# Performance work log

Measured on AMD Instinct MI355X. Metric: run time of the kernel, lower is better.

The kernel has to match this reference:

```python
import jax, jax.numpy as jnp
import numpy as np

B, S, HID = 1, 4096, 2048
HQ, HKV, D = 16, 8, 128
G = HQ // HKV
WINDOW = 1024
EPS = 1e-6
ROPE_THETA = 1e6


def setup_inputs() -> dict:
    key = jax.random.key(0)
    ks = jax.random.split(key, 6)
    hidden_states = jax.random.normal(ks[0], (B, S, HID), dtype=jnp.float32)
    Wq = jax.random.normal(ks[1], (HQ * D, HID), dtype=jnp.float32) * 0.02
    Wk = jax.random.normal(ks[2], (HKV * D, HID), dtype=jnp.float32) * 0.02
    Wv = jax.random.normal(ks[3], (HKV * D, HID), dtype=jnp.float32) * 0.02
    Wo = jax.random.normal(ks[4], (HID, HQ * D), dtype=jnp.float32) * 0.02
    q_norm_w = jnp.ones((D,), dtype=jnp.float32)
    k_norm_w = jnp.ones((D,), dtype=jnp.float32)
    # standard RoPE tables
    inv_freq = 1.0 / (ROPE_THETA ** (jnp.arange(0, D, 2, dtype=jnp.float32) / D))
    pos = jnp.arange(S, dtype=jnp.float32)
    freqs = pos[:, None] * inv_freq[None, :]            # [S, D/2]
    emb = jnp.concatenate([freqs, freqs], axis=-1)       # [S, D]
    cos = jnp.cos(emb)[None]                             # [1, S, D]
    sin = jnp.sin(emb)[None]
    return {"hidden_states": hidden_states, "cos": cos, "sin": sin,
            "Wq": Wq, "Wk": Wk, "Wv": Wv, "Wo": Wo,
            "q_norm_w": q_norm_w, "k_norm_w": k_norm_w}


def _rms_norm(x, w):
    var = jnp.mean(jnp.square(x), axis=-1, keepdims=True)
    return w * (x * jax.lax.rsqrt(var + EPS))


def _rotate_half(x):
    x1, x2 = jnp.split(x, 2, axis=-1)
    return jnp.concatenate([-x2, x1], axis=-1)


def reference(hidden_states, cos, sin, Wq, Wk, Wv, Wo, q_norm_w, k_norm_w):
    b, s, _ = hidden_states.shape
    # projections -> [B, H, S, D]
    q = (hidden_states @ Wq.T).reshape(b, s, HQ, D)
    k = (hidden_states @ Wk.T).reshape(b, s, HKV, D)
    v = (hidden_states @ Wv.T).reshape(b, s, HKV, D)
    q = _rms_norm(q, q_norm_w).transpose(0, 2, 1, 3)   # [B,HQ,S,D]
    k = _rms_norm(k, k_norm_w).transpose(0, 2, 1, 3)   # [B,HKV,S,D]
    v = v.transpose(0, 2, 1, 3)
    # RoPE (cos/sin broadcast over head dim)
    c = cos[:, None, :, :]
    sn = sin[:, None, :, :]
    q = q * c + _rotate_half(q) * sn
    k = k * c + _rotate_half(k) * sn
    # GQA: group queries per kv head
    qg = q.reshape(b, HKV, G, s, D)
    scaling = D ** -0.5
    scores = jnp.einsum('bhgqd,bhkd->bhgqk', qg, k) * scaling  # [B,HKV,G,S,S]
    # causal + sliding-window additive mask
    i = jnp.arange(s)[:, None]
    j = jnp.arange(s)[None, :]
    allowed = (j <= i) & (j > i - WINDOW)
    scores = jnp.where(allowed[None, None, None], scores, jnp.float32(-1e9))
    attn = jax.nn.softmax(scores, axis=-1)
    out = jnp.einsum('bhgqk,bhkd->bhgqd', attn, v)     # [B,HKV,G,S,D]
    out = out.reshape(b, HQ, s, D).transpose(0, 2, 1, 3).reshape(b, s, HQ * D)
    return out @ Wo.T
```

## Files before the change

### kernel.cpp

```cpp
#include <hip/hip_runtime.h>

typedef __bf16 bf16;
typedef bf16 bf16x8 __attribute__((ext_vector_type(8)));
typedef bf16 bf16x4 __attribute__((ext_vector_type(4)));
typedef float f32x4 __attribute__((ext_vector_type(4)));

#define MFMA16(a, b, c) __builtin_amdgcn_mfma_f32_16x16x32_bf16((a), (b), (c), 0, 0, 0)

__device__ __forceinline__ void gload_lds16(const bf16* g, bf16* l) {
  __builtin_amdgcn_global_load_lds(
      (const __attribute__((address_space(1))) void*)g,
      (__attribute__((address_space(3))) void*)l, 16, 0, 0);
}

template <int N>
__device__ __forceinline__ void lgkm_fence() {
  if constexpr (N == 0) asm volatile("s_waitcnt lgkmcnt(0)" ::: "memory");
  else if constexpr (N == 4) asm volatile("s_waitcnt lgkmcnt(4)" ::: "memory");
  else if constexpr (N == 8) asm volatile("s_waitcnt lgkmcnt(8)" ::: "memory");
  else if constexpr (N == 12) asm volatile("s_waitcnt lgkmcnt(12)" ::: "memory");
  __builtin_amdgcn_sched_barrier(0);
}
__device__ __forceinline__ void bar_fence() {
  __builtin_amdgcn_sched_barrier(0);
  __builtin_amdgcn_s_barrier();
}

__global__ __launch_bounds__(256) void cvt_f32_bf16(const float* __restrict__ src,
                                                    bf16* __restrict__ dst, int n4) {
  int i = blockIdx.x * blockDim.x + threadIdx.x;
  if (i < n4) {
    float4 v = ((const float4*)src)[i];
    bf16x4 o;
    o[0] = (bf16)v.x; o[1] = (bf16)v.y; o[2] = (bf16)v.z; o[3] = (bf16)v.w;
    ((bf16x4*)dst)[i] = o;
  }
}

template <int BM, int BN, int MT, int NTT, typename OutT>
__global__ __launch_bounds__(512, 2) void gemm_pipe(const bf16* __restrict__ A,
                                                    const bf16* __restrict__ B,
                                                    OutT* __restrict__ C,
                                                    int M, int N, int K) {
  constexpr int MH = MT / 2, NH = NTT / 2;
  constexpr int ASLOT = BM * 64;
  constexpr int BSLOT = BN * 64;
  constexpr int NLA = BM / 64, NLB = BN / 64;
  __shared__ __align__(16) bf16 SA[2 * ASLOT];
  __shared__ __align__(16) bf16 SB[2 * BSLOT];

  const int NTILES = K >> 6;
  const int tid = threadIdx.x;
  const int w = tid >> 6, lane = tid & 63;
  const int l15 = lane & 15, quad = lane >> 4;
  const int wr = w >> 2, wc = w & 3;

  const int nbx = N / BN;
  const int nwg = (M / BM) * nbx;
  const int wg = ((int)blockIdx.x & 7) * (nwg >> 3) + ((int)blockIdx.x >> 3);
  const int bm0 = (wg / nbx) * BM;
  const int bn0 = (wg % nbx) * BN;

  const int r0 = tid >> 3;
  const int sg = (tid & 7) ^ ((tid >> 3) & 7);
  unsigned aoffg[NLA], boffg[NLB];
#pragma unroll
  for (int i = 0; i < NLA; ++i)
    aoffg[i] = (unsigned)((bm0 + r0 + i * 64) * K + sg * 8);
#pragma unroll
  for (int i = 0; i < NLB; ++i)
    boffg[i] = (unsigned)((bn0 + r0 + i * 64) * K + sg * 8);

  const int xl = l15 & 7;
  const int p0 = quad ^ xl;
  const int baseA0 = (wr * (MT * 16) + l15) * 128 + p0 * 16;
  const int baseA1 = (wr * (MT * 16) + l15) * 128 + ((p0 ^ 4) * 16);
  const int baseB0 = (wc * (NTT * 16) + l15) * 128 + p0 * 16;
  const int baseB1 = (wc * (NTT * 16) + l15) * 128 + ((p0 ^ 4) * 16);
  const char* saB = (const char*)&SA[0];
  const char* sbB = (const char*)&SB[0];

  f32x4 acc[MT][NTT] = {};
  bf16x8 As[2][MH][2];
  bf16x8 Bs[2][NH][2];

#define LDA_(SL, H, DST)                                                        \
  _Pragma("unroll") for (int mt = 0; mt < MH; ++mt) {                           \
    (DST)[mt][0] = *(const bf16x8*)(saB + (SL) * (ASLOT * 2) + baseA0 +         \
                                    ((H) * MH + mt) * 2048);                    \
    (DST)[mt][1] = *(const bf16x8*)(saB + (SL) * (ASLOT * 2) + baseA1 +         \
                                    ((H) * MH + mt) * 2048);                    \
  }
#define LDB_(SL, G, DST)                                                        \
  _Pragma("unroll") for (int nt = 0; nt < NH; ++nt) {                           \
    (DST)[nt][0] = *(const bf16x8*)(sbB + (SL) * (BSLOT * 2) + baseB0 +         \
                                    ((G) * NH + nt) * 2048);                    \
    (DST)[nt][1] = *(const bf16x8*)(sbB + (SL) * (BSLOT * 2) + baseB1 +         \
                                    ((G) * NH + nt) * 2048);                    \
  }
#define QMFMA_(AS, BS, MHI, NHI)                                                \
  __builtin_amdgcn_s_setprio(1);                                                \
  _Pragma("unroll") for (int mt = 0; mt < MH; ++mt)                             \
      _Pragma("unroll") for (int nt = 0; nt < NH; ++nt) {                       \
    acc[(MHI) * MH + mt][(NHI) * NH + nt] = MFMA16(                             \
        (AS)[mt][0], (BS)[nt][0], acc[(MHI) * MH + mt][(NHI) * NH + nt]);       \
    acc[(MHI) * MH + mt][(NHI) * NH + nt] = MFMA16(                             \
        (AS)[mt][1], (BS)[nt][1], acc[(MHI) * MH + mt][(NHI) * NH + nt]);       \
  }                                                                             \
  __builtin_amdgcn_s_setprio(0);
#define STAGE_(SO, TS)                                                          \
  _Pragma("unroll") for (int i = 0; i < NLA; ++i)                               \
      gload_lds16(A + aoffg[i] + (TS) * 64, SA + (SO) * ASLOT + tid * 8 + i * 4096); \
  _Pragma("unroll") for (int i = 0; i < NLB; ++i)                               \
      gload_lds16(B + boffg[i] + (TS) * 64, SB + (SO) * BSLOT + tid * 8 + i * 4096);

#define GTILE_BODY(PAR, TS)                                                     \
  {                                                                             \
    constexpr int sl_ = (PAR), so_ = (PAR) ^ 1;                                 \
    constexpr int e0_ = (PAR), e1_ = (PAR) ^ 1;                                 \
                                                                        \
    LDB_(sl_, 1, Bs[e1_]);                                                      \
    bar_fence();                                                                \
    lgkm_fence<NTT>();                                                          \
    if ((TS) < NTILES) { STAGE_(so_, (TS)); }                                   \
    QMFMA_(As[0], Bs[e0_], 0, 0);                                               \
                                                                        \
    LDA_(sl_, 1, As[1]);                                                        \
    bar_fence();                                                                \
    lgkm_fence<MT>();                                                           \
    QMFMA_(As[0], Bs[e1_], 0, 1);                                               \
                                                                        \
    LDB_(sl_, 0, Bs[e0_]);                                                      \
    asm volatile("s_waitcnt vmcnt(0)" ::: "memory");                            \
    bar_fence();                                                                \
    lgkm_fence<NTT>();                                                          \
    QMFMA_(As[1], Bs[e1_], 1, 1);                                               \
                                                                        \
    LDA_(so_, 0, As[0]);                                                        \
    LDB_(so_, 0, Bs[e1_]);                                                      \
    bar_fence();                                                                \
    lgkm_fence<MT + NTT>();                                                     \
    QMFMA_(As[1], Bs[e0_], 1, 0);                                               \
  }

  { STAGE_(0, 0); }
  asm volatile("s_waitcnt vmcnt(0)" ::: "memory");
  bar_fence();
  __builtin_amdgcn_sched_barrier(0);
  LDA_(0, 0, As[0]);
  LDB_(0, 0, Bs[0]);

  for (int t = 0; t < NTILES; t += 2) {
    GTILE_BODY(0, t + 1);
    GTILE_BODY(1, t + 2);
  }

#undef LDA_
#undef LDB_
#undef QMFMA_
#undef STAGE_
#undef GTILE_BODY

#pragma unroll
  for (int mt = 0; mt < MT; ++mt)
#pragma unroll
    for (int nt = 0; nt < NTT; ++nt) {
      int row = bm0 + wr * (MT * 16) + mt * 16 + quad * 4;
      int col = bn0 + wc * (NTT * 16) + nt * 16 + l15;
#pragma unroll
      for (int r = 0; r < 4; ++r)
        C[(size_t)(row + r) * N + col] = (OutT)acc[mt][nt][r];
    }
}

__global__ __launch_bounds__(256) void normrope(const bf16* __restrict__ QKVb,
                                                const float* __restrict__ cosb,
                                                const float* __restrict__ sinb,
                                                const float* __restrict__ qw,
                                                const float* __restrict__ kw,
                                                bf16* __restrict__ Qb,
                                                bf16* __restrict__ Kb) {
  const int wid = (blockIdx.x * blockDim.x + threadIdx.x) >> 6;
  const int lane = threadIdx.x & 63;
  const int s = wid / 24;
  const int h = wid % 24;
  const bool isq = (h < 16);
  const int col0 = isq ? h * 128 : 2048 + (h - 16) * 128;
  const float* wt = isq ? qw : kw;

  const bf16* row = QKVb + (size_t)s * 4096 + col0;
  float x1 = (float)row[lane];
  float x2 = (float)row[lane + 64];

  float ss = x1 * x1 + x2 * x2;
#pragma unroll
  for (int m = 32; m >= 1; m >>= 1) ss += __shfl_xor(ss, m, 64);
  float rs = rsqrtf(ss * (1.0f / 128.0f) + 1e-6f);

  float c = cosb[(size_t)s * 128 + lane];
  float sn = sinb[(size_t)s * 128 + lane];
  float xn1 = x1 * rs * wt[lane];
  float xn2 = x2 * rs * wt[lane + 64];
  float o1 = xn1 * c - xn2 * sn;
  float o2 = xn2 * c + xn1 * sn;
  const float scale = isq ? 0.12751652f : 1.0f;
  o1 *= scale; o2 *= scale;

  bf16* dst = isq ? (Qb + ((size_t)h * 4096 + s) * 128)
                  : (Kb + ((size_t)(h - 16) * 4096 + s) * 128);
  dst[lane] = (bf16)o1;
  dst[lane + 64] = (bf16)o2;
}

__global__ __launch_bounds__(256) void vtrans(const bf16* __restrict__ QKVb,
                                              bf16* __restrict__ Vtp) {
  __shared__ __align__(16) bf16 T[64 * 136];
  const int kvh = blockIdx.y;
  const int s0 = blockIdx.x * 64;
  const int tid = threadIdx.x;
  for (int g = tid; g < 1024; g += 256) {
    int s = g >> 4, cg = g & 15;
    *(bf16x8*)(T + s * 136 + cg * 8) =
        *(const bf16x8*)(QKVb + (size_t)(s0 + s) * 4096 + 3072 + kvh * 128 + cg * 8);
  }
  __syncthreads();
  for (int g = tid; g < 1024; g += 256) {
    int d = g >> 3, sg = g & 7;
    bf16x8 v;
#pragma unroll
    for (int j = 0; j < 8; j++) {
      int kp = sg * 8 + j;
      int s = (kp & 3) * 16 + (kp >> 2);
      v[j] = T[s * 136 + d];
    }
    *(bf16x8*)(Vtp + ((size_t)kvh * 128 + d) * 4096 + s0 + sg * 8) = v;
  }
}

__global__ __launch_bounds__(256, 2) void attn_kernel(const bf16* __restrict__ Qb,
                                                      const bf16* __restrict__ Kb,
                                                      const bf16* __restrict__ Vtp,
                                                      bf16* __restrict__ Ob) {
  const int SEQ = 4096, W = 1024;
  const float MP = 17.312340f;
  __shared__ __align__(16) bf16 Ks[64 * 128];
  __shared__ __align__(16) bf16 Vs[128 * 64];
  __shared__ __align__(16) bf16 Ps[4][32 * 64];

  const int id = blockIdx.x;
  const int kvh = id & 7, gq = (id >> 3) & 1, h = kvh * 2 + gq;
  const int qb0 = (id >> 4) * 128;
  const int tid = threadIdx.x, w = tid >> 6, lane = tid & 63;
  const int l15 = lane & 15, quad = lane >> 4;
  const int qw0 = qb0 + w * 32;

  bf16x8 qf[2][4];
#pragma unroll
  for (int m = 0; m < 2; m++) {
    const bf16* qp = Qb + ((size_t)h * SEQ + qw0 + m * 16 + l15) * 128 + quad * 8;
#pragma unroll
    for (int kb = 0; kb < 4; kb++) qf[m][kb] = *(const bf16x8*)(qp + kb * 32);
  }

  f32x4 o[2][8] = {};
  f32x4 lr[2] = {};
  bf16* pw = &Ps[w][0];
  const bf16* kbase = Kb + (size_t)kvh * SEQ * 128;
  const bf16* vbase = Vtp + (size_t)kvh * 128 * SEQ;

  int jmin = qb0 - (W - 1); if (jmin < 0) jmin = 0;
  const int kt0 = jmin >> 6, kt1 = (qb0 + 127) >> 6;

  for (int kt = kt0; kt <= kt1; ++kt) {
    const int k0 = kt * 64;
#pragma unroll
    for (int i = 0; i < 4; i++) {
      int slot = w * 256 + i * 64 + lane;
      int key = slot >> 4, gg = slot & 15;
      int gsw = gg ^ (key & 7);
      gload_lds16(kbase + (size_t)(k0 + key) * 128 + gsw * 8, Ks + (w * 256 + i * 64) * 8);
    }
#pragma unroll
    for (int i = 0; i < 4; i++) {
      int slot = w * 256 + i * 64 + lane;
      int d = slot >> 3, gg = slot & 7;
      int gsw = gg ^ (d & 7);
      gload_lds16(vbase + (size_t)d * SEQ + k0 + gsw * 8, Vs + (w * 256 + i * 64) * 8);
    }
    __syncthreads();

    const bool alive = (k0 <= qw0 + 31) && (k0 + 63 > qw0 - W);
    if (alive) {
      const bool full = (k0 + 63 <= qw0) && (k0 > qw0 + 31 - W);
      f32x4 s[2][4] = {};
#pragma unroll
      for (int c = 0; c < 4; c++) {
        const int key = c * 16 + l15;
        bf16x8 kf[4];
#pragma unroll
        for (int kb = 0; kb < 4; kb++)
          kf[kb] = *(const bf16x8*)(Ks + key * 128 + (((kb * 4 + quad) ^ (key & 7)) << 3));
#pragma unroll
        for (int kb = 0; kb < 4; kb++) {
          s[0][c] = MFMA16(qf[0][kb], kf[kb], s[0][c]);
          s[1][c] = MFMA16(qf[1][kb], kf[kb], s[1][c]);
        }
      }
#pragma unroll
      for (int m = 0; m < 2; m++)
#pragma unroll
        for (int r = 0; r < 4; r++) {
          float p[4];
          if (full) {
#pragma unroll
            for (int c = 0; c < 4; c++) p[c] = __builtin_amdgcn_exp2f(s[m][c][r] - MP);
          } else {
            const int i_ = qw0 + m * 16 + quad * 4 + r;
#pragma unroll
            for (int c = 0; c < 4; c++) {
              int j = k0 + c * 16 + l15;
              p[c] = (j <= i_ && j > i_ - W) ? __builtin_amdgcn_exp2f(s[m][c][r] - MP) : 0.0f;
            }
          }
          lr[m][r] += p[0] + p[1] + p[2] + p[3];
          bf16x4 pk;
          pk[0] = (bf16)p[0]; pk[1] = (bf16)p[1]; pk[2] = (bf16)p[2]; pk[3] = (bf16)p[3];
          const int qrow = m * 16 + quad * 4 + r;
          *(bf16x4*)(pw + qrow * 64 + (((l15 >> 1) ^ (qrow & 7)) << 3) + (l15 & 1) * 4) = pk;
        }
      asm volatile("s_waitcnt lgkmcnt(0)" ::: "memory");
      bf16x8 pf[2][2];
#pragma unroll
      for (int m = 0; m < 2; m++)
#pragma unroll
        for (int kb = 0; kb < 2; kb++)
          pf[m][kb] = *(const bf16x8*)(pw + (m * 16 + l15) * 64 +
                                       (((kb * 4 + quad) ^ (l15 & 7)) << 3));
#pragma unroll
      for (int n = 0; n < 8; n++) {
        const int d = n * 16 + l15;
        bf16x8 vf0 = *(const bf16x8*)(Vs + d * 64 + ((quad ^ (l15 & 7)) << 3));
        bf16x8 vf1 = *(const bf16x8*)(Vs + d * 64 + (((4 + quad) ^ (l15 & 7)) << 3));
        o[0][n] = MFMA16(pf[0][0], vf0, o[0][n]);
        o[0][n] = MFMA16(pf[0][1], vf1, o[0][n]);
        o[1][n] = MFMA16(pf[1][0], vf0, o[1][n]);
        o[1][n] = MFMA16(pf[1][1], vf1, o[1][n]);
      }
    }
    __syncthreads();
  }

  float linv[2][4];
#pragma unroll
  for (int m = 0; m < 2; m++)
#pragma unroll
    for (int r = 0; r < 4; r++) {
      float v = lr[m][r];
      v += __shfl_xor(v, 1, 64);
      v += __shfl_xor(v, 2, 64);
      v += __shfl_xor(v, 4, 64);
      v += __shfl_xor(v, 8, 64);
      linv[m][r] = 1.0f / v;
    }
#pragma unroll
  for (int m = 0; m < 2; m++)
#pragma unroll
    for (int n = 0; n < 8; n++)
#pragma unroll
      for (int r = 0; r < 4; r++) {
        int i_ = qw0 + m * 16 + quad * 4 + r;
        Ob[(size_t)i_ * 2048 + h * 128 + n * 16 + l15] = (bf16)(o[m][n][r] * linv[m][r]);
      }
}

extern "C" void kernel_launch(void* const* d_in, const int* in_sizes, int n_in,
                              void* d_out, int out_size, void* d_ws, size_t ws_size,
                              hipStream_t stream) {
  const float* hid  = (const float*)d_in[0];
  const float* cosb = (const float*)d_in[1];
  const float* sinb = (const float*)d_in[2];
  const float* Wq   = (const float*)d_in[3];
  const float* Wk   = (const float*)d_in[4];
  const float* Wv   = (const float*)d_in[5];
  const float* Wo   = (const float*)d_in[6];
  const float* qw   = (const float*)d_in[7];
  const float* kw   = (const float*)d_in[8];

  if (ws_size < (size_t)(112u) * 1024u * 1024u) return;

  char* ws = (char*)d_ws;
  bf16* Xbf  = (bf16*)(ws);
  bf16* Vtp  = (bf16*)(ws);
  bf16* Wcat = (bf16*)(ws + (16u << 20));
  bf16* Wob  = (bf16*)(ws + (32u << 20));
  bf16* QKVb = (bf16*)(ws + (40u << 20));
  bf16* Qb   = (bf16*)(ws + (72u << 20));
  bf16* Kb   = (bf16*)(ws + (88u << 20));
  bf16* Ob   = (bf16*)(ws + (96u << 20));

  cvt_f32_bf16<<<8192, 256, 0, stream>>>(hid, Xbf, 2097152);
  cvt_f32_bf16<<<4096, 256, 0, stream>>>(Wq, Wcat, 1048576);
  cvt_f32_bf16<<<2048, 256, 0, stream>>>(Wk, Wcat + 4194304, 524288);
  cvt_f32_bf16<<<2048, 256, 0, stream>>>(Wv, Wcat + 6291456, 524288);
  cvt_f32_bf16<<<4096, 256, 0, stream>>>(Wo, Wob, 1048576);

  gemm_pipe<256, 256, 8, 4, bf16><<<256, 512, 0, stream>>>(Xbf, Wcat, QKVb, 4096, 4096, 2048);
  vtrans<<<dim3(64, 8), 256, 0, stream>>>(QKVb, Vtp);
  normrope<<<24576, 256, 0, stream>>>(QKVb, cosb, sinb, qw, kw, Qb, Kb);
  attn_kernel<<<512, 256, 0, stream>>>(Qb, Kb, Vtp, Ob);
  gemm_pipe<128, 256, 4, 4, float><<<256, 512, 0, stream>>>(Ob, Wob, (float*)d_out, 4096, 2048, 2048);
}
```

Before: 325.4 us.

## Double-buffer K/V tiles in attention with 512-thread blocks and MFMA priority

The attention kernel now uses 512-thread blocks covering 256 queries each, with half as many blocks. K/V tiles are double-buffered in LDS and the next tile is prefetched asynchronously while the current one is computed, with waits on vmcnt in place of full syncthreads. s_setprio is raised around the MFMA blocks. Each loaded K/V tile is reused by more query rows, but LDS use per block doubles and only 256 blocks run on a 256-CU GPU, so occupancy may drop.

```diff
diff --git a/kernel.cpp b/kernel.cpp
--- a/kernel.cpp
+++ b/kernel.cpp
@@ -237,19 +237,19 @@
   }
 }
 
-__global__ __launch_bounds__(256, 2) void attn_kernel(const bf16* __restrict__ Qb,
+__global__ __launch_bounds__(512, 1) void attn_kernel(const bf16* __restrict__ Qb,
                                                       const bf16* __restrict__ Kb,
                                                       const bf16* __restrict__ Vtp,
                                                       bf16* __restrict__ Ob) {
   const int SEQ = 4096, W = 1024;
   const float MP = 17.312340f;
-  __shared__ __align__(16) bf16 Ks[64 * 128];
-  __shared__ __align__(16) bf16 Vs[128 * 64];
-  __shared__ __align__(16) bf16 Ps[4][32 * 64];
+  __shared__ __align__(16) bf16 Ks[2][64 * 128];
+  __shared__ __align__(16) bf16 Vs[2][128 * 64];
+  __shared__ __align__(16) bf16 Ps[8][32 * 64];
 
   const int id = blockIdx.x;
   const int kvh = id & 7, gq = (id >> 3) & 1, h = kvh * 2 + gq;
-  const int qb0 = (id >> 4) * 128;
+  const int qb0 = (id >> 4) * 256;
   const int tid = threadIdx.x, w = tid >> 6, lane = tid & 63;
   const int l15 = lane & 15, quad = lane >> 4;
   const int qw0 = qb0 + w * 32;
@@ -269,26 +269,42 @@
   const bf16* vbase = Vtp + (size_t)kvh * 128 * SEQ;
 
   int jmin = qb0 - (W - 1); if (jmin < 0) jmin = 0;
-  const int kt0 = jmin >> 6, kt1 = (qb0 + 127) >> 6;
+  const int kt0 = jmin >> 6, kt1 = (qb0 + 255) >> 6;
+
+#define ASTAGE(KT, SL)                                                          \
+  do {                                                                          \
+    const int k0_ = (KT) * 64;                                                  \
+    _Pragma("unroll") for (int i_ = 0; i_ < 2; ++i_) {                          \
+      int slot = i_ * 512 + tid;                                                \
+      int key = slot >> 4, gg = slot & 15;                                      \
+      int gsw = gg ^ (key & 7);                                                 \
+      gload_lds16(kbase + (size_t)(k0_ + key) * 128 + gsw * 8,                  \
+                  &Ks[SL][0] + slot * 8);                                       \
+    }                                                                           \
+    _Pragma("unroll") for (int i_ = 0; i_ < 2; ++i_) {                          \
+      int slot = i_ * 512 + tid;                                                \
+      int d = slot >> 3, gg = slot & 7;                                         \
+      int gsw = gg ^ (d & 7);                                                   \
+      gload_lds16(vbase + (size_t)d * SEQ + k0_ + gsw * 8,                      \
+                  &Vs[SL][0] + slot * 8);                                       \
+    }                                                                           \
+  } while (0)
+
+  ASTAGE(kt0, 0);
 
   for (int kt = kt0; kt <= kt1; ++kt) {
+    const int sl = (kt - kt0) & 1;
+    if (kt < kt1) {
+      ASTAGE(kt + 1, sl ^ 1);
+      asm volatile("s_waitcnt vmcnt(4)" ::: "memory");
+    } else {
+      asm volatile("s_waitcnt vmcnt(0)" ::: "memory");
+    }
+    __builtin_amdgcn_s_barrier();
+
     const int k0 = kt * 64;
-#pragma unroll
-    for (int i = 0; i < 4; i++) {
-      int slot = w * 256 + i * 64 + lane;
-      int key = slot >> 4, gg = slot & 15;
-      int gsw = gg ^ (key & 7);
-      gload_lds16(kbase + (size_t)(k0 + key) * 128 + gsw * 8, Ks + (w * 256 + i * 64) * 8);
-    }
-#pragma unroll
-    for (int i = 0; i < 4; i++) {
-      int slot = w * 256 + i * 64 + lane;
-      int d = slot >> 3, gg = slot & 7;
-      int gsw = gg ^ (d & 7);
-      gload_lds16(vbase + (size_t)d * SEQ + k0 + gsw * 8, Vs + (w * 256 + i * 64) * 8);
-    }
-    __syncthreads();
-
+    const bf16* ks = &Ks[sl][0];
+    const bf16* vs = &Vs[sl][0];
     const bool alive = (k0 <= qw0 + 31) && (k0 + 63 > qw0 - W);
     if (alive) {
       const bool full = (k0 + 63 <= qw0) && (k0 > qw0 + 31 - W);
@@ -299,12 +315,14 @@
         bf16x8 kf[4];
 #pragma unroll
         for (int kb = 0; kb < 4; kb++)
-          kf[kb] = *(const bf16x8*)(Ks + key * 128 + (((kb * 4 + quad) ^ (key & 7)) << 3));
+          kf[kb] = *(const bf16x8*)(ks + key * 128 + (((kb * 4 + quad) ^ (key & 7)) << 3));
+        __builtin_amdgcn_s_setprio(1);
 #pragma unroll
         for (int kb = 0; kb < 4; kb++) {
           s[0][c] = MFMA16(qf[0][kb], kf[kb], s[0][c]);
           s[1][c] = MFMA16(qf[1][kb], kf[kb], s[1][c]);
         }
+        __builtin_amdgcn_s_setprio(0);
       }
 #pragma unroll
       for (int m = 0; m < 2; m++)
@@ -339,16 +357,19 @@
 #pragma unroll
       for (int n = 0; n < 8; n++) {
         const int d = n * 16 + l15;
-        bf16x8 vf0 = *(const bf16x8*)(Vs + d * 64 + ((quad ^ (l15 & 7)) << 3));
-        bf16x8 vf1 = *(const bf16x8*)(Vs + d * 64 + (((4 + quad) ^ (l15 & 7)) << 3));
+        bf16x8 vf0 = *(const bf16x8*)(vs + d * 64 + ((quad ^ (l15 & 7)) << 3));
+        bf16x8 vf1 = *(const bf16x8*)(vs + d * 64 + (((4 + quad) ^ (l15 & 7)) << 3));
+        __builtin_amdgcn_s_setprio(1);
         o[0][n] = MFMA16(pf[0][0], vf0, o[0][n]);
         o[0][n] = MFMA16(pf[0][1], vf1, o[0][n]);
         o[1][n] = MFMA16(pf[1][0], vf0, o[1][n]);
         o[1][n] = MFMA16(pf[1][1], vf1, o[1][n]);
+        __builtin_amdgcn_s_setprio(0);
       }
     }
-    __syncthreads();
-  }
+    __builtin_amdgcn_s_barrier();
+  }
+#undef ASTAGE
 
   float linv[2][4];
 #pragma unroll
@@ -407,6 +428,6 @@
   gemm_pipe<256, 256, 8, 4, bf16><<<256, 512, 0, stream>>>(Xbf, Wcat, QKVb, 4096, 4096, 2048);
   vtrans<<<dim3(64, 8), 256, 0, stream>>>(QKVb, Vtp);
   normrope<<<24576, 256, 0, stream>>>(QKVb, cosb, sinb, qw, kw, Qb, Kb);
-  attn_kernel<<<512, 256, 0, stream>>>(Qb, Kb, Vtp, Ob);
+  attn_kernel<<<256, 512, 0, stream>>>(Qb, Kb, Vtp, Ob);
   gemm_pipe<128, 256, 4, 4, float><<<256, 512, 0, stream>>>(Ob, Wob, (float*)d_out, 4096, 2048, 2048);
 }
```

Result: no change. 329.5 us (+1.3%).
